# Optimization experiments

Measured on AMD Instinct MI355X. Metric: run time of the kernel, lower is better.

Reference implementation:

```python
import jax, jax.numpy as jnp
import numpy as np

N = 4096
IN_DIM = 6
HID = 32
HEADS1 = 4
OUT_DIM = 64


def _gat_layer(x, mask, W, a_src, a_dst, b):
    # x: [n, in], W: [in, heads*d], a_src/a_dst: [heads, d], b: [heads*d]
    n = x.shape[0]
    heads, d = a_src.shape
    h = (x @ W).reshape(n, heads, d)                      # [n, heads, d]
    e_src = jnp.einsum('nhd,hd->nh', h, a_src)            # [n, heads]
    e_dst = jnp.einsum('nhd,hd->nh', h, a_dst)            # [n, heads]
    logits = e_src[:, None, :] + e_dst[None, :, :]        # [n, n, heads]
    logits = jax.nn.leaky_relu(logits, negative_slope=0.2)
    logits = jnp.where(mask[:, :, None], logits, jnp.float32(-1e9))
    alpha = jax.nn.softmax(logits, axis=1)                # softmax over j (dim=1)
    # dropout disabled (eval mode reference)
    out = jnp.einsum('ijh,jhd->ihd', alpha, h).reshape(n, heads * d)
    return out + b


def setup_inputs() -> dict:
    key = jax.random.key(0)
    ks = jax.random.split(key, 10)
    x = jax.random.normal(ks[0], (N, IN_DIM), dtype=jnp.float32)
    adj = jax.random.bernoulli(ks[1], 0.01, (N, N)).astype(jnp.float32)
    s = 0.1
    W1 = jax.random.normal(ks[2], (IN_DIM, HEADS1 * HID), dtype=jnp.float32) * s
    a_src1 = jax.random.normal(ks[3], (HEADS1, HID), dtype=jnp.float32) * s
    a_dst1 = jax.random.normal(ks[4], (HEADS1, HID), dtype=jnp.float32) * s
    b1 = jnp.zeros((HEADS1 * HID,), dtype=jnp.float32)
    W2 = jax.random.normal(ks[5], (HEADS1 * HID, OUT_DIM), dtype=jnp.float32) * s
    a_src2 = jax.random.normal(ks[6], (1, OUT_DIM), dtype=jnp.float32) * s
    a_dst2 = jax.random.normal(ks[7], (1, OUT_DIM), dtype=jnp.float32) * s
    b2 = jnp.zeros((OUT_DIM,), dtype=jnp.float32)
    return {'x': x, 'adj': adj, 'W1': W1, 'a_src1': a_src1, 'a_dst1': a_dst1,
            'b1': b1, 'W2': W2, 'a_src2': a_src2, 'a_dst2': a_dst2, 'b2': b2}


def reference(x, adj, W1, a_src1, a_dst1, b1, W2, a_src2, a_dst2, b2):
    n = x.shape[0]
    # add self loops: a = max(a, I), mask = a > 0
    a = jnp.maximum(adj, jnp.eye(n, dtype=adj.dtype))
    mask = a > 0
    h1 = jax.nn.elu(_gat_layer(x, mask, W1, a_src1, a_dst1, b1))
    # dropout disabled (eval mode)
    h2 = _gat_layer(h1, mask, W2, a_src2, a_dst2, b2)
    return h2
```

## Files before the change

### kernel.cpp

```cpp
#include <hip/hip_runtime.h>

#define N 4096
#define IN_DIM 6
#define HEADS1 4
#define D1 128
#define OUT_DIM 64
#define MAXNB 192
#define LGS 200

#define WFENCE() do { asm volatile("s_waitcnt lgkmcnt(0)" ::: "memory"); \
                      __builtin_amdgcn_sched_barrier(0); } while (0)

__device__ __forceinline__ float lrelu(float v) { return v > 0.f ? v : 0.2f * v; }
__device__ __forceinline__ float selh(float4 v, int h) {
    return (h == 0) ? v.x : (h == 1) ? v.y : (h == 2) ? v.z : v.w;
}

__global__ __launch_bounds__(256) void kA(
    const float* __restrict__ x,  const float* __restrict__ W1,
    const float* __restrict__ a_src1, const float* __restrict__ a_dst1,
    const float* __restrict__ W2,
    float* __restrict__ hpre, float* __restrict__ es1, float* __restrict__ ed1,
    float* __restrict__ W2T)
{
    int w = threadIdx.x >> 6, l = threadIdx.x & 63;
    int i = blockIdx.x * 4 + w;

    float xv[IN_DIM];
    #pragma unroll
    for (int k = 0; k < IN_DIM; ++k) xv[k] = x[i*IN_DIM + k];

    float a0 = 0.f, a1 = 0.f;
    #pragma unroll
    for (int k = 0; k < IN_DIM; ++k) {
        float2 wv = ((const float2*)W1)[k*64 + l];
        a0 += xv[k] * wv.x;
        a1 += xv[k] * wv.y;
    }
    float2 hv; hv.x = a0; hv.y = a1;
    ((float2*)hpre)[(size_t)i*64 + l] = hv;

    float2 asv = ((const float2*)a_src1)[l];
    float2 adv = ((const float2*)a_dst1)[l];
    float ps = a0*asv.x + a1*asv.y;
    float pd = a0*adv.x + a1*adv.y;
    #pragma unroll
    for (int off = 8; off >= 1; off >>= 1) {
        ps += __shfl_xor(ps, off, 64);
        pd += __shfl_xor(pd, off, 64);
    }
    if ((l & 15) == 0) {
        int h = l >> 4;
        es1[i*HEADS1 + h] = ps;
        ed1[i*HEADS1 + h] = pd;
    }

    if (blockIdx.x == 0) {
        for (int idx = threadIdx.x; idx < D1*OUT_DIM; idx += 256) {
            int k = idx >> 6, o = idx & 63;
            W2T[o*D1 + k] = W2[idx];
        }
    }
}

__global__ __launch_bounds__(256, 4) void kB(
    const float* __restrict__ adj,  const float* __restrict__ hpre,
    const float* __restrict__ es1,  const float* __restrict__ ed1,
    const float* __restrict__ b1,   const float* __restrict__ W2T,
    const float* __restrict__ a_src2, const float* __restrict__ a_dst2,
    int* __restrict__ cnt, int* __restrict__ idxg,
    float* __restrict__ h2pre, float* __restrict__ es2, float* __restrict__ ed2)
{
    __shared__ int   jsS[4][MAXNB];
    __shared__ float lgS[4][HEADS1][LGS];
    __shared__ float h1S[4][D1];
    int w = threadIdx.x >> 6, l = threadIdx.x & 63;
    int i = blockIdx.x * 4 + w;
    int*   js  = jsS[w];
    float (*lg)[LGS] = lgS[w];
    float* h1s = h1S[w];

    const float4* row = (const float4*)(adj + (size_t)i * N);
    float4 buf[16];
    #pragma unroll
    for (int u = 0; u < 16; ++u) buf[u] = row[l + 64*u];
    __builtin_amdgcn_sched_barrier(0);

    unsigned long long lanem = (1ull << l) - 1ull;
    int base = 0;
    #pragma unroll
    for (int u = 0; u < 16; ++u) {
        float fe[4] = {buf[u].x, buf[u].y, buf[u].z, buf[u].w};
        #pragma unroll
        for (int e = 0; e < 4; ++e) {
            int j = (64*u + l)*4 + e;
            bool pred = (fe[e] > 0.f) || (j == i);
            unsigned long long mask = __ballot(pred);
            if (pred) {
                int pos = base + (int)__popcll(mask & lanem);
                if (pos < MAXNB) js[pos] = j;
            }
            base += (int)__popcll(mask);
        }
    }
    int c = min(base, MAXNB);
    if (l == 0) cnt[i] = c;
    WFENCE();

    float4 esv = ((const float4*)es1)[i];
    float4 lr0, lr1, lr2;
    lr0.x = lr0.y = lr0.z = lr0.w = -1e30f; lr1 = lr0; lr2 = lr0;
    if (l < c) {
        int j = js[l];
        float4 e4 = ((const float4*)ed1)[j];
        lr0.x = lrelu(esv.x + e4.x); lr0.y = lrelu(esv.y + e4.y);
        lr0.z = lrelu(esv.z + e4.z); lr0.w = lrelu(esv.w + e4.w);
        idxg[i*MAXNB + l] = j;
    }
    if (l + 64 < c) {
        int p = l + 64, j = js[p];
        float4 e4 = ((const float4*)ed1)[j];
        lr1.x = lrelu(esv.x + e4.x); lr1.y = lrelu(esv.y + e4.y);
        lr1.z = lrelu(esv.z + e4.z); lr1.w = lrelu(esv.w + e4.w);
        idxg[i*MAXNB + p] = j;
    }
    if (l + 128 < c) {
        int p = l + 128, j = js[p];
        float4 e4 = ((const float4*)ed1)[j];
        lr2.x = lrelu(esv.x + e4.x); lr2.y = lrelu(esv.y + e4.y);
        lr2.z = lrelu(esv.z + e4.z); lr2.w = lrelu(esv.w + e4.w);
        idxg[i*MAXNB + p] = j;
    }

    float4 mm;
    mm.x = fmaxf(lr0.x, fmaxf(lr1.x, lr2.x));
    mm.y = fmaxf(lr0.y, fmaxf(lr1.y, lr2.y));
    mm.z = fmaxf(lr0.z, fmaxf(lr1.z, lr2.z));
    mm.w = fmaxf(lr0.w, fmaxf(lr1.w, lr2.w));
    #pragma unroll
    for (int off = 32; off >= 1; off >>= 1) {
        mm.x = fmaxf(mm.x, __shfl_xor(mm.x, off, 64));
        mm.y = fmaxf(mm.y, __shfl_xor(mm.y, off, 64));
        mm.z = fmaxf(mm.z, __shfl_xor(mm.z, off, 64));
        mm.w = fmaxf(mm.w, __shfl_xor(mm.w, off, 64));
    }
    float4 ex0, ex1, ex2;
    ex0.x = __expf(lr0.x-mm.x); ex0.y = __expf(lr0.y-mm.y);
    ex0.z = __expf(lr0.z-mm.z); ex0.w = __expf(lr0.w-mm.w);
    ex1.x = __expf(lr1.x-mm.x); ex1.y = __expf(lr1.y-mm.y);
    ex1.z = __expf(lr1.z-mm.z); ex1.w = __expf(lr1.w-mm.w);
    ex2.x = __expf(lr2.x-mm.x); ex2.y = __expf(lr2.y-mm.y);
    ex2.z = __expf(lr2.z-mm.z); ex2.w = __expf(lr2.w-mm.w);
    float4 ss;
    ss.x = ex0.x + ex1.x + ex2.x;
    ss.y = ex0.y + ex1.y + ex2.y;
    ss.z = ex0.z + ex1.z + ex2.z;
    ss.w = ex0.w + ex1.w + ex2.w;
    #pragma unroll
    for (int off = 32; off >= 1; off >>= 1) {
        ss.x += __shfl_xor(ss.x, off, 64);
        ss.y += __shfl_xor(ss.y, off, 64);
        ss.z += __shfl_xor(ss.z, off, 64);
        ss.w += __shfl_xor(ss.w, off, 64);
    }
    float4 iv; iv.x = 1.f/ss.x; iv.y = 1.f/ss.y; iv.z = 1.f/ss.z; iv.w = 1.f/ss.w;
    lg[0][l]     = ex0.x*iv.x; lg[1][l]     = ex0.y*iv.y;
    lg[2][l]     = ex0.z*iv.z; lg[3][l]     = ex0.w*iv.w;
    lg[0][l+64]  = ex1.x*iv.x; lg[1][l+64]  = ex1.y*iv.y;
    lg[2][l+64]  = ex1.z*iv.z; lg[3][l+64]  = ex1.w*iv.w;
    lg[0][l+128] = ex2.x*iv.x; lg[1][l+128] = ex2.y*iv.y;
    lg[2][l+128] = ex2.z*iv.z; lg[3][l+128] = ex2.w*iv.w;
    WFENCE();

    int hl = l >> 4;
    const float2* hp2 = (const float2*)hpre;
    float ax = 0.f, ay = 0.f;
    int p = 0;
    for (; p + 8 <= c; p += 8) {
        int   jj[8]; float ww[8];
        #pragma unroll
        for (int u = 0; u < 8; ++u) jj[u] = js[p+u];
        #pragma unroll
        for (int u = 0; u < 8; ++u) ww[u] = lg[hl][p+u];
        #pragma unroll
        for (int u = 0; u < 8; ++u) {
            float2 v = hp2[(size_t)jj[u]*64 + l];
            ax += ww[u]*v.x; ay += ww[u]*v.y;
        }
    }
    for (; p < c; ++p) {
        float wv = lg[hl][p];
        float2 v = hp2[(size_t)js[p]*64 + l];
        ax += wv*v.x; ay += wv*v.y;
    }
    float2 bv = ((const float2*)b1)[l];
    float v0 = ax + bv.x, v1 = ay + bv.y;
    v0 = (v0 > 0.f) ? v0 : expm1f(v0);
    v1 = (v1 > 0.f) ? v1 : expm1f(v1);
    { float2 hw; hw.x = v0; hw.y = v1; *(float2*)(h1s + 2*l) = hw; }
    WFENCE();

    const float4* wrow = (const float4*)(W2T + (size_t)l*D1);
    float h2 = 0.f;
    #pragma unroll 8
    for (int k4 = 0; k4 < 32; ++k4) {
        float4 wv = wrow[k4];
        float4 hvv = *(const float4*)(h1s + k4*4);
        h2 += wv.x*hvv.x + wv.y*hvv.y + wv.z*hvv.z + wv.w*hvv.w;
    }
    h2pre[(size_t)i*OUT_DIM + l] = h2;
    float ps = h2 * a_src2[l];
    float pd = h2 * a_dst2[l];
    #pragma unroll
    for (int off = 32; off >= 1; off >>= 1) {
        ps += __shfl_xor(ps, off, 64);
        pd += __shfl_xor(pd, off, 64);
    }
    if (l == 0) { es2[i] = ps; ed2[i] = pd; }
}

__global__ __launch_bounds__(256, 4) void kC(
    const float* __restrict__ h2pre, const float* __restrict__ es2,
    const float* __restrict__ ed2,   const int* __restrict__ cnt,
    const int* __restrict__ idxg,    const float* __restrict__ b2v,
    float* __restrict__ out)
{
    __shared__ int   jsS[4][MAXNB];
    __shared__ float alS[4][MAXNB];
    int w = threadIdx.x >> 6, l = threadIdx.x & 63;
    int i = blockIdx.x * 4 + w;
    int*   js = jsS[w];
    float* al = alS[w];
    int c = cnt[i];
    float esi = es2[i];

    float l0 = -1e30f, l1 = -1e30f, l2 = -1e30f;
    if (l < c) {
        int j = idxg[i*MAXNB + l];             js[l] = j;
        l0 = lrelu(esi + ed2[j]);
    }
    if (l + 64 < c) {
        int p = l + 64, j = idxg[i*MAXNB + p]; js[p] = j;
        l1 = lrelu(esi + ed2[j]);
    }
    if (l + 128 < c) {
        int p = l + 128, j = idxg[i*MAXNB + p]; js[p] = j;
        l2 = lrelu(esi + ed2[j]);
    }
    float m = fmaxf(l0, fmaxf(l1, l2));
    #pragma unroll
    for (int off = 32; off >= 1; off >>= 1) m = fmaxf(m, __shfl_xor(m, off, 64));
    float e0 = __expf(l0-m), e1 = __expf(l1-m), e2 = __expf(l2-m);
    float s = e0 + e1 + e2;
    #pragma unroll
    for (int off = 32; off >= 1; off >>= 1) s += __shfl_xor(s, off, 64);
    float inv = 1.f / s;
    al[l]     = e0*inv;
    al[l+64]  = e1*inv;
    al[l+128] = e2*inv;
    WFENCE();

    float acc = 0.f;
    int p = 0;
    for (; p + 8 <= c; p += 8) {
        int   jj[8]; float ww[8];
        #pragma unroll
        for (int u = 0; u < 8; ++u) jj[u] = js[p+u];
        #pragma unroll
        for (int u = 0; u < 8; ++u) ww[u] = al[p+u];
        #pragma unroll
        for (int u = 0; u < 8; ++u)
            acc += ww[u] * h2pre[(size_t)jj[u]*OUT_DIM + l];
    }
    for (; p < c; ++p)
        acc += al[p] * h2pre[(size_t)js[p]*OUT_DIM + l];
    out[(size_t)i*OUT_DIM + l] = acc + b2v[l];
}

extern "C" void kernel_launch(void* const* d_in, const int* in_sizes, int n_in,
                              void* d_out, int out_size, void* d_ws, size_t ws_size,
                              hipStream_t stream) {
    const float* x      = (const float*)d_in[0];
    const float* adj    = (const float*)d_in[1];
    const float* W1     = (const float*)d_in[2];
    const float* a_src1 = (const float*)d_in[3];
    const float* a_dst1 = (const float*)d_in[4];
    const float* b1     = (const float*)d_in[5];
    const float* W2     = (const float*)d_in[6];
    const float* a_src2 = (const float*)d_in[7];
    const float* a_dst2 = (const float*)d_in[8];
    const float* b2v    = (const float*)d_in[9];
    float* out = (float*)d_out;

    float* ws    = (float*)d_ws;
    float* hpre  = ws;
    float* h2pre = hpre  + (size_t)N*D1;
    float* es1   = h2pre + (size_t)N*OUT_DIM;
    float* ed1   = es1   + (size_t)N*HEADS1;
    float* es2   = ed1   + (size_t)N*HEADS1;
    float* ed2   = es2   + N;
    float* W2T   = ed2   + N;
    int*   cnt   = (int*)(W2T + OUT_DIM*D1);
    int*   idxg  = cnt + N;

    kA<<<N/4, 256, 0, stream>>>(x, W1, a_src1, a_dst1, W2, hpre, es1, ed1, W2T);
    kB<<<N/4, 256, 0, stream>>>(adj, hpre, es1, ed1, b1, W2T, a_src2, a_dst2,
                                cnt, idxg, h2pre, es2, ed2);
    kC<<<N/4, 256, 0, stream>>>(h2pre, es2, ed2, cnt, idxg, b2v, out);
}
```

Before: 144.7 us.

## Stage adjacency rows into LDS via global_load_lds with one wave per block

Kernel kB now runs one 64-thread wave per block, one row each, instead of four waves per block. Each adjacency row is loaded straight from global memory into a 16 KB LDS stage buffer with global_load_lds, and the compaction loop then reads it back from LDS. This drops the 16 float4 register buffer, lowering register pressure and possibly raising occupancy. In exchange it adds LDS traffic, and the 16 KB per single-wave block may limit how many blocks fit on a CU.

```diff
diff --git a/kernel.cpp b/kernel.cpp
--- a/kernel.cpp
+++ b/kernel.cpp
@@ -10,11 +10,14 @@
 
 #define WFENCE() do { asm volatile("s_waitcnt lgkmcnt(0)" ::: "memory"); \
                       __builtin_amdgcn_sched_barrier(0); } while (0)
+#define VFENCE() do { asm volatile("s_waitcnt vmcnt(0)" ::: "memory"); \
+                      __builtin_amdgcn_sched_barrier(0); } while (0)
+#define GLOAD_LDS16(gp, lp) \
+    __builtin_amdgcn_global_load_lds( \
+        (const __attribute__((address_space(1))) void*)(gp), \
+        (__attribute__((address_space(3))) void*)(lp), 16, 0, 0)
 
 __device__ __forceinline__ float lrelu(float v) { return v > 0.f ? v : 0.2f * v; }
-__device__ __forceinline__ float selh(float4 v, int h) {
-    return (h == 0) ? v.x : (h == 1) ? v.y : (h == 2) ? v.z : v.w;
-}
 
 __global__ __launch_bounds__(256) void kA(
     const float* __restrict__ x,  const float* __restrict__ W1,
@@ -63,7 +66,7 @@
     }
 }
 
-__global__ __launch_bounds__(256, 4) void kB(
+__global__ __launch_bounds__(64, 4) void kB(
     const float* __restrict__ adj,  const float* __restrict__ hpre,
     const float* __restrict__ es1,  const float* __restrict__ ed1,
     const float* __restrict__ b1,   const float* __restrict__ W2T,
@@ -71,26 +74,26 @@
     int* __restrict__ cnt, int* __restrict__ idxg,
     float* __restrict__ h2pre, float* __restrict__ es2, float* __restrict__ ed2)
 {
-    __shared__ int   jsS[4][MAXNB];
-    __shared__ float lgS[4][HEADS1][LGS];
-    __shared__ float h1S[4][D1];
-    int w = threadIdx.x >> 6, l = threadIdx.x & 63;
-    int i = blockIdx.x * 4 + w;
-    int*   js  = jsS[w];
-    float (*lg)[LGS] = lgS[w];
-    float* h1s = h1S[w];
-
-    const float4* row = (const float4*)(adj + (size_t)i * N);
-    float4 buf[16];
-    #pragma unroll
-    for (int u = 0; u < 16; ++u) buf[u] = row[l + 64*u];
-    __builtin_amdgcn_sched_barrier(0);
+    __shared__ float stage[N];
+    __shared__ int   js[MAXNB];
+    __shared__ float lg[HEADS1][LGS];
+    __shared__ float h1s[D1];
+    int l = threadIdx.x;
+    int i = blockIdx.x;
+
+    const float* gbase = adj + (size_t)i * N + l*4;
+    #pragma unroll
+    for (int u = 0; u < 16; ++u)
+        GLOAD_LDS16(gbase + u*256, &stage[u*256]);
+    VFENCE();
 
     unsigned long long lanem = (1ull << l) - 1ull;
+    const float4* st4 = (const float4*)stage;
     int base = 0;
-    #pragma unroll
+    #pragma unroll 4
     for (int u = 0; u < 16; ++u) {
-        float fe[4] = {buf[u].x, buf[u].y, buf[u].z, buf[u].w};
+        float4 v = st4[l + 64*u];
+        float fe[4] = {v.x, v.y, v.z, v.w};
         #pragma unroll
         for (int e = 0; e < 4; ++e) {
             int j = (64*u + l)*4 + e;
@@ -304,7 +307,7 @@
     int*   idxg  = cnt + N;
 
     kA<<<N/4, 256, 0, stream>>>(x, W1, a_src1, a_dst1, W2, hpre, es1, ed1, W2T);
-    kB<<<N/4, 256, 0, stream>>>(adj, hpre, es1, ed1, b1, W2T, a_src2, a_dst2,
+    kB<<<N,    64, 0, stream>>>(adj, hpre, es1, ed1, b1, W2T, a_src2, a_dst2,
                                 cnt, idxg, h2pre, es2, ed2);
     kC<<<N/4, 256, 0, stream>>>(h2pre, es2, ed2, cnt, idxg, b2v, out);
 }
```

After: 159.1 us. +10.0%, slower.
